# Optimization experiments

Hardware: AMD Instinct MI355X
Metric: run time of the kernel (lower is better)

The kernel has to match this reference:

```python
import jax, jax.numpy as jnp
import numpy as np
from jax import lax

C_OUT = 32   # out_capsules[0]
D_OUT = 8    # out_capsules[1]
ROUTING_ITERS = 3
EPS = 1e-8


def squash(s):
    # squash over capsule-channel axis c (dim 1 of B c d h w)
    n2 = jnp.sum(s * s, axis=1, keepdims=True)
    return s * (n2 / (1.0 + n2)) / jnp.sqrt(n2 + EPS)


def setup_inputs() -> dict:
    key = jax.random.key(0)
    k1, k2 = jax.random.split(key)
    x = jax.random.normal(k1, (8, 16, 8, 96, 96), dtype=jnp.float32)
    # torch Conv3d weight layout: (out_ch, in_ch, kD, kH, kW); scaled ~ kaiming-ish
    w_conv = jax.random.normal(k2, (C_OUT * D_OUT, 16, 1, 3, 3), dtype=jnp.float32) * 0.05
    return {"x": x, "w_conv": w_conv}


def reference(x, w_conv):
    # Conv3d, no bias, valid padding, stride 1, kernel (1,3,3)
    u = lax.conv_general_dilated(
        x, w_conv, window_strides=(1, 1, 1), padding='VALID',
        dimension_numbers=('NCDHW', 'OIDHW', 'NCDHW'))  # (B, c*d, D, h, w)
    B, _, D, h, w = u.shape
    # rearrange 'B (c d) D h w -> B c D d h w'
    u = u.reshape(B, C_OUT, D_OUT, D, h, w).transpose(0, 1, 3, 2, 4, 5)

    b = jnp.zeros((B, D, D_OUT, h, w), dtype=u.dtype)
    s = None
    for _ in range(ROUTING_ITERS):
        # softmax_3d: exp normalized over (d, h, w), keeping D
        e = jnp.exp(b)
        c = e / jnp.sum(e, axis=(2, 3, 4), keepdims=True)
        s = jnp.einsum('BDdhw,BcDdhw->Bcdhw', c, u)
        b = b + jnp.einsum('BcDdhw,Bcdhw->BDdhw', u, squash(s))
    return s
```

## Files before the change

kernel.cpp:

```cpp
#include <hip/hip_runtime.h>
#include <math.h>

#define CIN   16
#define DDEP  8
#define HIN   96
#define WIN   96
#define HOUT  94
#define WOUT  94
#define HW    (HOUT*WOUT)
#define CH    256
#define DCAP  8
#define KTOT  (CIN*9)
#define KTILES 5
#define APAD  168
#define EPSQ  1e-8f

#define B_ELEMS ((size_t)8*DDEP*DCAP*HW)
#define WFRAG_ELEMS ((size_t)KTILES*16*64*8)
#define VSITES (DCAP*HW)
#define NBLK2  277
#define XN ((size_t)8*CIN*DDEP*HIN*WIN)
#define G_BYTES ((size_t)8*VSITES*36*4)

typedef __attribute__((ext_vector_type(8))) short bf16x8;
typedef __attribute__((ext_vector_type(4))) float f32x4;

__device__ __forceinline__ ushort f2bf(float f) {
    unsigned u = __float_as_uint(f);
    return (ushort)((u + 0x7FFFu + ((u >> 16) & 1u)) >> 16);
}
__device__ __forceinline__ float bf2f(ushort h) {
    return __uint_as_float(((unsigned)h) << 16);
}

__global__ __launch_bounds__(64) void build_wfrag(
    const float* __restrict__ w, ushort* __restrict__ w_hi, ushort* __restrict__ w_lo)
{
    const int lane = threadIdx.x;
    const int nt = blockIdx.x, kt = blockIdx.y;
    const int n  = nt*16 + (lane & 15);
    const int kb = kt*32 + (lane >> 4)*8;
    size_t off = (((size_t)kt*16 + nt)*64 + lane)*8;
    for (int j = 0; j < 8; ++j) {
        int k = kb + j;
        float v = (k < KTOT) ? w[(size_t)n*KTOT + k] : 0.f;
        ushort hi = f2bf(v);
        float  r  = v - bf2f(hi);
        ushort lo = f2bf(r);
        w_hi[off + j] = hi; w_lo[off + j] = lo;
    }
}

__global__ __launch_bounds__(256) void xconvert(
    const float* __restrict__ x, ushort* __restrict__ xb)
{
    size_t i = (size_t)blockIdx.x*256 + threadIdx.x;
    if (i*4 >= XN) return;
    float4 v = ((const float4*)x)[i];
    ushort4 o;
    o.x = f2bf(v.x); o.y = f2bf(v.y); o.z = f2bf(v.z); o.w = f2bf(v.w);
    ((ushort4*)xb)[i] = o;
}

__global__ __launch_bounds__(256) void zreduce(
    const float* __restrict__ Zp, float* __restrict__ Z, int dst, int count)
{
    const int bd = blockIdx.x;
    const float* p = Zp + (size_t)bd * count;
    float s = 0.f;
    for (int i = threadIdx.x; i < count; i += 256) s += p[i];
    #pragma unroll
    for (int off = 1; off < 64; off <<= 1) s += __shfl_xor(s, off);
    __shared__ float ps[4];
    if ((threadIdx.x & 63) == 0) ps[threadIdx.x >> 6] = s;
    __syncthreads();
    if (threadIdx.x == 0) Z[dst + bd] = ps[0] + ps[1] + ps[2] + ps[3];
}

__global__ __launch_bounds__(256, 2) void conv_g(
    const ushort* __restrict__ xb,
    const ushort* __restrict__ w_hi, const ushort* __restrict__ w_lo,
    float* __restrict__ Gm)
{
    const int t  = threadIdx.x;
    const int wx = blockIdx.x, h0 = blockIdx.y, bb = blockIdx.z;
    const int w0 = wx*8;

    __shared__ __align__(16) ushort a_hi[64][APAD];
    __shared__ union {
        ushort patchb[CIN][DDEP][3][10];
        float gst[4][16][36];
    } ov;

    for (int i = t; i < CIN*DDEP*3*5; i += 256) {
        int ci = i / 120, rem = i - ci*120;
        int D  = rem / 15, r2 = rem - D*15;
        int kh = r2 / 5, uc = r2 - kh*5;
        int xc = w0 + uc*2;
        const ushort* row = xb + (((size_t)(bb*CIN + ci)*DDEP + D)*HIN + (h0+kh))*WIN;
        unsigned v;
        if (xc + 1 < WIN) v = *(const unsigned*)&row[xc];
        else { unsigned e = row[95]; v = e | (e << 16); }
        *(unsigned*)&ov.patchb[ci][D][kh][uc*2] = v;
    }
    __syncthreads();

    {
        const int site = t >> 2, kg = t & 3;
        const int D = site >> 3, wi = site & 7;
        #pragma unroll
        for (int u2 = 0; u2 < 18; ++u2) {
            int k0 = kg*36 + u2*2;
            int ci0 = k0/9, r0 = k0 - ci0*9, kh0 = r0/3, kw0 = r0 - kh0*3;
            int k1 = k0 + 1;
            int ci1 = k1/9, r1 = k1 - ci1*9, kh1 = r1/3, kw1 = r1 - kh1*3;
            unsigned lo = ov.patchb[ci0][D][kh0][wi+kw0];
            unsigned hi = ov.patchb[ci1][D][kh1][wi+kw1];
            *(unsigned*)&a_hi[site][k0] = lo | (hi << 16);
        }
        if (t < 64) {
            #pragma unroll
            for (int kk = KTOT; kk < KTILES*32; kk += 2)
                *(unsigned*)&a_hi[t][kk] = 0u;
        }
    }
    __syncthreads();

    const int wv = t >> 6, lane = t & 63;
    const int m16 = lane & 15, quad = lane >> 4;
    const int Dq  = quad >> 1;
    const int wih = quad & 1;
    f32x4 acc[4][4];
    #pragma unroll
    for (int mt = 0; mt < 4; ++mt)
        #pragma unroll
        for (int nt = 0; nt < 4; ++nt)
            acc[mt][nt] = (f32x4){0.f, 0.f, 0.f, 0.f};

    #pragma unroll
    for (int kt = 0; kt < KTILES; ++kt) {
        bf16x8 ah[4];
        #pragma unroll
        for (int mt = 0; mt < 4; ++mt)
            ah[mt] = *(const bf16x8*)&a_hi[mt*16 + m16][kt*32 + quad*8];
        #pragma unroll
        for (int nt = 0; nt < 4; ++nt) {
            size_t off = (((size_t)kt*16 + (wv*4 + nt))*64 + lane)*8;
            bf16x8 bh = *(const bf16x8*)&w_hi[off];
            bf16x8 bl = *(const bf16x8*)&w_lo[off];
            #pragma unroll
            for (int mt = 0; mt < 4; ++mt) {
                acc[mt][nt] = __builtin_amdgcn_mfma_f32_16x16x32_bf16(ah[mt], bh, acc[mt][nt], 0, 0, 0);
                acc[mt][nt] = __builtin_amdgcn_mfma_f32_16x16x32_bf16(ah[mt], bl, acc[mt][nt], 0, 0, 0);
            }
        }
    }

    {
        const int c3 = m16 >> 3;
        const int dL = m16 & 7;
        __syncthreads();
        #pragma unroll
        for (int r = 0; r < 4; ++r) {
            const int rq = r >> 1;
            float G36[36];
            #pragma unroll
            for (int j = 0; j < 36; ++j) G36[j] = 0.f;
            #pragma unroll
            for (int nt = 0; nt < 4; ++nt) {
                float u8[8];
                #pragma unroll
                for (int mt = 0; mt < 4; ++mt) {
                    float own = acc[mt][nt][r];
                    float oth = __shfl_xor(own, 32);
                    if (Dq == 0) { u8[mt*2]   = own; u8[mt*2+1] = oth; }
                    else         { u8[mt*2+1] = own; u8[mt*2]   = oth; }
                }
                if (Dq == rq) {
                    int idx = 0;
                    #pragma unroll
                    for (int D = 0; D < 8; ++D)
                        #pragma unroll
                        for (int Dp = D; Dp < 8; ++Dp) {
                            G36[idx] += u8[D]*u8[Dp];
                            ++idx;
                        }
                }
            }
            if (Dq == rq) {
                #pragma unroll
                for (int j = 0; j < 36; ++j) G36[j] += __shfl_xor(G36[j], 8);
                if (c3 == 0) {
                    #pragma unroll
                    for (int j = 0; j < 36; ++j) ov.gst[wv][dL*2 + wih][j] = G36[j];
                }
            }
            __syncthreads();
            for (int idx2 = t; idx2 < 16*36; idx2 += 256) {
                int sidx = idx2 / 36, j = idx2 - sidx*36;
                int dd = sidx >> 1, wh = sidx & 1;
                int w = w0 + wh*4 + r;
                if (w < WOUT) {
                    float gv = ov.gst[0][sidx][j] + ov.gst[1][sidx][j]
                             + ov.gst[2][sidx][j] + ov.gst[3][sidx][j];
                    size_t gsite = ((size_t)(bb*DCAP + dd)*HOUT + h0)*WOUT + w;
                    Gm[gsite*36 + j] = gv;
                }
            }
            __syncthreads();
        }
    }
}

template<int ITER>
__global__ __launch_bounds__(256) void gram_route(
    const float* __restrict__ Gm, float* __restrict__ bws,
    const float* __restrict__ Z, float* __restrict__ Zp)
{
    const int k = blockIdx.x, bb = blockIdx.y;
    const int t = threadIdx.x;
    const int local = k*256 + t;
    const bool valid = local < VSITES;
    float ez8[8];
    #pragma unroll
    for (int D = 0; D < 8; ++D) ez8[D] = 0.f;
    if (valid) {
        const int d  = local / HW;
        const int r2 = local - d*HW;
        float bv[8], cm[8];
        if (ITER == 1) {
            const float inv = 1.0f / (float)(DCAP * HW);
            #pragma unroll
            for (int D = 0; D < 8; ++D) { bv[D] = 0.f; cm[D] = inv; }
        } else {
            #pragma unroll
            for (int D = 0; D < 8; ++D) {
                bv[D] = bws[((size_t)(bb*64 + D*8 + d))*HW + r2];
                cm[D] = expf(bv[D]) * (1.0f / Z[bb*8 + D]);
            }
        }
        float g[36];
        const float4* gp = (const float4*)(Gm + (size_t)(bb*VSITES + local)*36);
        #pragma unroll
        for (int q = 0; q < 9; ++q) {
            float4 v = gp[q];
            g[q*4+0] = v.x; g[q*4+1] = v.y; g[q*4+2] = v.z; g[q*4+3] = v.w;
        }
        float tD[8];
        #pragma unroll
        for (int D = 0; D < 8; ++D) tD[D] = 0.f;
        {
            int idx = 0;
            #pragma unroll
            for (int D = 0; D < 8; ++D)
                #pragma unroll
                for (int Dp = D; Dp < 8; ++Dp) {
                    float gv = g[idx]; ++idx;
                    tD[D] += cm[Dp] * gv;
                    if (Dp != D) tD[Dp] += cm[D] * gv;
                }
        }
        float n2 = 0.f;
        #pragma unroll
        for (int D = 0; D < 8; ++D) n2 += cm[D] * tD[D];
        float fac = (n2 / (1.f + n2)) / sqrtf(n2 + EPSQ);
        #pragma unroll
        for (int D = 0; D < 8; ++D) {
            float nb = bv[D] + fac * tD[D];
            bws[((size_t)(bb*64 + D*8 + d))*HW + r2] = nb;
            ez8[D] = expf(nb);
        }
    }
    #pragma unroll
    for (int D = 0; D < 8; ++D)
        #pragma unroll
        for (int off = 1; off < 64; off <<= 1) ez8[D] += __shfl_xor(ez8[D], off);
    __shared__ float ps[4][8];
    if ((t & 63) == 0) {
        #pragma unroll
        for (int D = 0; D < 8; ++D) ps[t >> 6][D] = ez8[D];
    }
    __syncthreads();
    if (t < 8)
        Zp[((size_t)bb*8 + t)*NBLK2 + k] = ps[0][t] + ps[1][t] + ps[2][t] + ps[3][t];
}

__global__ __launch_bounds__(256, 2) void conv_s(
    const ushort* __restrict__ xb,
    const ushort* __restrict__ w_hi, const ushort* __restrict__ w_lo,
    const float* __restrict__ bws, const float* __restrict__ Z,
    float* __restrict__ out)
{
    const int t  = threadIdx.x;
    const int wx = blockIdx.x, h0 = blockIdx.y, bb = blockIdx.z;
    const int w0 = wx*8;

    __shared__ __align__(16) ushort a_hi[64][APAD];
    __shared__ float  cms[64][8];
    __shared__ float  invZ[8];
    __shared__ union {
        ushort patchb[CIN][DDEP][3][10];
        float  sout[256][8];
    } ov;

    if (t < 8) invZ[t] = 1.0f / Z[64 + bb*8 + t];
    for (int v = t; v < 512; v += 256) {
        int Dd = v >> 3, wi = v & 7;
        int w = w0 + wi;
        float bv = (w < WOUT) ? bws[((size_t)bb*64 + Dd)*HW + (size_t)h0*WOUT + w] : 0.f;
        cms[Dd][wi] = expf(bv);
    }
    for (int i = t; i < CIN*DDEP*3*5; i += 256) {
        int ci = i / 120, rem = i - ci*120;
        int D  = rem / 15, r2 = rem - D*15;
        int kh = r2 / 5, uc = r2 - kh*5;
        int xc = w0 + uc*2;
        const ushort* row = xb + (((size_t)(bb*CIN + ci)*DDEP + D)*HIN + (h0+kh))*WIN;
        unsigned v;
        if (xc + 1 < WIN) v = *(const unsigned*)&row[xc];
        else { unsigned e = row[95]; v = e | (e << 16); }
        *(unsigned*)&ov.patchb[ci][D][kh][uc*2] = v;
    }
    __syncthreads();

    {
        const int site = t >> 2, kg = t & 3;
        const int D = site >> 3, wi = site & 7;
        #pragma unroll
        for (int u2 = 0; u2 < 18; ++u2) {
            int k0 = kg*36 + u2*2;
            int ci0 = k0/9, r0 = k0 - ci0*9, kh0 = r0/3, kw0 = r0 - kh0*3;
            int k1 = k0 + 1;
            int ci1 = k1/9, r1 = k1 - ci1*9, kh1 = r1/3, kw1 = r1 - kh1*3;
            unsigned lo = ov.patchb[ci0][D][kh0][wi+kw0];
            unsigned hi = ov.patchb[ci1][D][kh1][wi+kw1];
            *(unsigned*)&a_hi[site][k0] = lo | (hi << 16);
        }
        if (t < 64) {
            #pragma unroll
            for (int kk = KTOT; kk < KTILES*32; kk += 2)
                *(unsigned*)&a_hi[t][kk] = 0u;
        }
    }
    __syncthreads();

    const int wv = t >> 6, lane = t & 63;
    const int m16 = lane & 15, quad = lane >> 4;
    f32x4 acc[4][4];
    #pragma unroll
    for (int mt = 0; mt < 4; ++mt)
        #pragma unroll
        for (int nt = 0; nt < 4; ++nt)
            acc[mt][nt] = (f32x4){0.f, 0.f, 0.f, 0.f};

    #pragma unroll
    for (int kt = 0; kt < KTILES; ++kt) {
        bf16x8 ah[4];
        #pragma unroll
        for (int mt = 0; mt < 4; ++mt)
            ah[mt] = *(const bf16x8*)&a_hi[mt*16 + m16][kt*32 + quad*8];
        #pragma unroll
        for (int nt = 0; nt < 4; ++nt) {
            size_t off = (((size_t)kt*16 + (wv*4 + nt))*64 + lane)*8;
            bf16x8 bh = *(const bf16x8*)&w_hi[off];
            bf16x8 bl = *(const bf16x8*)&w_lo[off];
            #pragma unroll
            for (int mt = 0; mt < 4; ++mt) {
                acc[mt][nt] = __builtin_amdgcn_mfma_f32_16x16x32_bf16(ah[mt], bh, acc[mt][nt], 0, 0, 0);
                acc[mt][nt] = __builtin_amdgcn_mfma_f32_16x16x32_bf16(ah[mt], bl, acc[mt][nt], 0, 0, 0);
            }
        }
    }

    const int d   = m16 & 7;
    const int Dq  = quad >> 1;
    const int wih = quad & 1;
    float svv[4][4];
    {
        float cmw[4][4];
        #pragma unroll
        for (int mt = 0; mt < 4; ++mt) {
            int D = mt*2 + Dq;
            float iz = invZ[D];
            #pragma unroll
            for (int r = 0; r < 4; ++r) cmw[mt][r] = cms[D*8 + d][wih*4 + r] * iz;
        }
        #pragma unroll
        for (int nt = 0; nt < 4; ++nt)
            #pragma unroll
            for (int r = 0; r < 4; ++r) {
                float partial = 0.f;
                #pragma unroll
                for (int mt = 0; mt < 4; ++mt) partial += cmw[mt][r]*acc[mt][nt][r];
                partial += __shfl_xor(partial, 32);
                svv[nt][r] = partial;
            }
    }
    if (quad < 2) {
        #pragma unroll
        for (int nt = 0; nt < 4; ++nt) {
            int ch = wv*64 + nt*16 + m16;
            #pragma unroll
            for (int r = 0; r < 4; ++r) ov.sout[ch][wih*4 + r] = svv[nt][r];
        }
    }
    __syncthreads();
    for (int i = t; i < 1024; i += 256) {
        int c2 = i >> 2, wip = i & 3;
        int w = w0 + wip*2;
        if (w + 1 < WOUT) {
            float2 v2 = { ov.sout[c2][wip*2], ov.sout[c2][wip*2 + 1] };
            *(float2*)&out[((size_t)bb*CH + c2)*HW + (size_t)h0*WOUT + w] = v2;
        }
    }
}

extern "C" void kernel_launch(void* const* d_in, const int* in_sizes, int n_in,
                              void* d_out, int out_size, void* d_ws, size_t ws_size,
                              hipStream_t stream)
{
    (void)in_sizes; (void)n_in; (void)out_size; (void)ws_size;
    const float* x     = (const float*)d_in[0];
    const float* wconv = (const float*)d_in[1];
    float* out = (float*)d_out;

    float*  bws  = (float*)d_ws;
    float*  Z    = bws + B_ELEMS;
    float*  Zp   = Z + 128;
    ushort* w_hi = (ushort*)(Zp + 64*NBLK2);
    ushort* w_lo = w_hi + WFRAG_ELEMS;
    ushort* xb   = w_lo + WFRAG_ELEMS;
    size_t  base = (size_t)((char*)(xb + XN) - (char*)d_ws);
    size_t  goff = (base + 255) & ~(size_t)255;
    float*  Gm   = (float*)((char*)d_ws + goff);

    const dim3 grid(12, 94, 8);
    build_wfrag<<<dim3(16, KTILES), 64, 0, stream>>>(wconv, w_hi, w_lo);
    xconvert<<<(unsigned)(XN/4/256), 256, 0, stream>>>(x, xb);
    conv_g<<<grid, 256, 0, stream>>>(xb, w_hi, w_lo, Gm);
    gram_route<1><<<dim3(NBLK2, 8), 256, 0, stream>>>(Gm, bws, Z, Zp);
    zreduce<<<64, 256, 0, stream>>>(Zp, Z, 0, NBLK2);
    gram_route<2><<<dim3(NBLK2, 8), 256, 0, stream>>>(Gm, bws, Z, Zp);
    zreduce<<<64, 256, 0, stream>>>(Zp, Z, 64, NBLK2);
    conv_s<<<grid, 256, 0, stream>>>(xb, w_hi, w_lo, bws, Z, out);
}
```

Baseline: 564.1 us.

## Fuse first routing iteration into conv_g and fold Z reductions into consumers

Merges the weight-fragment build and x-to-bf16 conversion into one prep kernel. Computes the first routing update (uniform coupling) inside conv_g from the per-site Gram values already in shared memory, and writes b and per-block exp partial sums there. This removes one full gram_route pass over Gm. The zreduce kernels are dropped; each consumer block re-sums the partials itself. The cost is redundant partial-sum reads in every block, plus extra per-block work and shared memory in conv_g.

```diff
diff --git a/kernel.cpp b/kernel.cpp
--- a/kernel.cpp
+++ b/kernel.cpp
@@ -17,9 +17,11 @@
 
 #define B_ELEMS ((size_t)8*DDEP*DCAP*HW)
 #define WFRAG_ELEMS ((size_t)KTILES*16*64*8)
+#define BLK_PER_B (94*12)
 #define VSITES (DCAP*HW)
 #define NBLK2  277
 #define XN ((size_t)8*CIN*DDEP*HIN*WIN)
+#define XBLK  9216
 #define G_BYTES ((size_t)8*VSITES*36*4)
 
 typedef __attribute__((ext_vector_type(8))) short bf16x8;
@@ -33,54 +35,39 @@
     return __uint_as_float(((unsigned)h) << 16);
 }
 
-__global__ __launch_bounds__(64) void build_wfrag(
+__global__ __launch_bounds__(256) void prep(
+    const float* __restrict__ x, ushort* __restrict__ xb,
     const float* __restrict__ w, ushort* __restrict__ w_hi, ushort* __restrict__ w_lo)
 {
-    const int lane = threadIdx.x;
-    const int nt = blockIdx.x, kt = blockIdx.y;
-    const int n  = nt*16 + (lane & 15);
-    const int kb = kt*32 + (lane >> 4)*8;
-    size_t off = (((size_t)kt*16 + nt)*64 + lane)*8;
-    for (int j = 0; j < 8; ++j) {
-        int k = kb + j;
-        float v = (k < KTOT) ? w[(size_t)n*KTOT + k] : 0.f;
-        ushort hi = f2bf(v);
-        float  r  = v - bf2f(hi);
-        ushort lo = f2bf(r);
-        w_hi[off + j] = hi; w_lo[off + j] = lo;
-    }
-}
-
-__global__ __launch_bounds__(256) void xconvert(
-    const float* __restrict__ x, ushort* __restrict__ xb)
-{
-    size_t i = (size_t)blockIdx.x*256 + threadIdx.x;
-    if (i*4 >= XN) return;
-    float4 v = ((const float4*)x)[i];
-    ushort4 o;
-    o.x = f2bf(v.x); o.y = f2bf(v.y); o.z = f2bf(v.z); o.w = f2bf(v.w);
-    ((ushort4*)xb)[i] = o;
-}
-
-__global__ __launch_bounds__(256) void zreduce(
-    const float* __restrict__ Zp, float* __restrict__ Z, int dst, int count)
-{
-    const int bd = blockIdx.x;
-    const float* p = Zp + (size_t)bd * count;
-    float s = 0.f;
-    for (int i = threadIdx.x; i < count; i += 256) s += p[i];
-    #pragma unroll
-    for (int off = 1; off < 64; off <<= 1) s += __shfl_xor(s, off);
-    __shared__ float ps[4];
-    if ((threadIdx.x & 63) == 0) ps[threadIdx.x >> 6] = s;
-    __syncthreads();
-    if (threadIdx.x == 0) Z[dst + bd] = ps[0] + ps[1] + ps[2] + ps[3];
+    const int bid = blockIdx.x;
+    if (bid < XBLK) {
+        size_t i = (size_t)bid*256 + threadIdx.x;
+        float4 v = ((const float4*)x)[i];
+        ushort4 o;
+        o.x = f2bf(v.x); o.y = f2bf(v.y); o.z = f2bf(v.z); o.w = f2bf(v.w);
+        ((ushort4*)xb)[i] = o;
+    } else if (threadIdx.x < 64) {
+        const int b2 = bid - XBLK;
+        const int nt = b2 & 15, kt = b2 >> 4;
+        const int lane = threadIdx.x;
+        const int n  = nt*16 + (lane & 15);
+        const int kb = kt*32 + (lane >> 4)*8;
+        size_t off = (((size_t)kt*16 + nt)*64 + lane)*8;
+        for (int j = 0; j < 8; ++j) {
+            int k = kb + j;
+            float v = (k < KTOT) ? w[(size_t)n*KTOT + k] : 0.f;
+            ushort hi = f2bf(v);
+            float  r  = v - bf2f(hi);
+            ushort lo = f2bf(r);
+            w_hi[off + j] = hi; w_lo[off + j] = lo;
+        }
+    }
 }
 
 __global__ __launch_bounds__(256, 2) void conv_g(
     const ushort* __restrict__ xb,
     const ushort* __restrict__ w_hi, const ushort* __restrict__ w_lo,
-    float* __restrict__ Gm)
+    float* __restrict__ bws, float* __restrict__ Zp1, float* __restrict__ Gm)
 {
     const int t  = threadIdx.x;
     const int wx = blockIdx.x, h0 = blockIdx.y, bb = blockIdx.z;
@@ -91,6 +78,7 @@
         ushort patchb[CIN][DDEP][3][10];
         float gst[4][16][36];
     } ov;
+    __shared__ float b1s[8][8][8];
 
     for (int i = t; i < CIN*DDEP*3*5; i += 256) {
         int ci = i / 120, rem = i - ci*120;
@@ -207,18 +195,78 @@
                     Gm[gsite*36 + j] = gv;
                 }
             }
+            if (t < 16) {
+                const int sdd = t >> 1, swh = t & 1;
+                const int sw = w0 + swh*4 + r;
+                if (sw < WOUT) {
+                    const float inv = 1.0f / (float)(DCAP * HW);
+                    float g36[36];
+                    #pragma unroll
+                    for (int j = 0; j < 36; ++j)
+                        g36[j] = ov.gst[0][t][j] + ov.gst[1][t][j]
+                               + ov.gst[2][t][j] + ov.gst[3][t][j];
+                    float tD[8];
+                    #pragma unroll
+                    for (int D = 0; D < 8; ++D) tD[D] = 0.f;
+                    int idx = 0;
+                    #pragma unroll
+                    for (int D = 0; D < 8; ++D)
+                        #pragma unroll
+                        for (int Dp = D; Dp < 8; ++Dp) {
+                            float gv = g36[idx]; ++idx;
+                            tD[D] += inv * gv;
+                            if (Dp != D) tD[Dp] += inv * gv;
+                        }
+                    float n2 = 0.f;
+                    #pragma unroll
+                    for (int D = 0; D < 8; ++D) n2 += inv * tD[D];
+                    float fac = (n2 / (1.f + n2)) / sqrtf(n2 + EPSQ);
+                    #pragma unroll
+                    for (int D = 0; D < 8; ++D) b1s[sdd][swh*4 + r][D] = fac * tD[D];
+                }
+            }
             __syncthreads();
         }
     }
-}
-
-template<int ITER>
-__global__ __launch_bounds__(256) void gram_route(
+
+    {
+        int Dd = t >> 2, wip = t & 3;
+        int D = Dd >> 3, d2 = Dd & 7;
+        int w = w0 + wip*2;
+        float ez = 0.f;
+        if (w + 1 < WOUT) {
+            float2 add;
+            add.x = b1s[d2][wip*2][D];
+            add.y = b1s[d2][wip*2 + 1][D];
+            *(float2*)&bws[((size_t)bb*64 + Dd)*HW + (size_t)h0*WOUT + w] = add;
+            ez = expf(add.x) + expf(add.y);
+        }
+        #pragma unroll
+        for (int off = 1; off < 32; off <<= 1) ez += __shfl_xor(ez, off);
+        if ((t & 31) == 0)
+            Zp1[((size_t)bb*8 + D)*BLK_PER_B + h0*12 + wx] = ez;
+    }
+}
+
+__global__ __launch_bounds__(256) void gram_route2(
     const float* __restrict__ Gm, float* __restrict__ bws,
-    const float* __restrict__ Z, float* __restrict__ Zp)
+    const float* __restrict__ Zp1, float* __restrict__ Zp2)
 {
     const int k = blockIdx.x, bb = blockIdx.y;
     const int t = threadIdx.x;
+
+    __shared__ float invZ1[8];
+    {
+        const int Dg = t >> 5;
+        const float* p = Zp1 + ((size_t)bb*8 + Dg)*BLK_PER_B;
+        float s = 0.f;
+        for (int k2 = (t & 31); k2 < BLK_PER_B; k2 += 32) s += p[k2];
+        #pragma unroll
+        for (int off = 1; off < 32; off <<= 1) s += __shfl_xor(s, off);
+        if ((t & 31) == 0) invZ1[Dg] = 1.0f / s;
+    }
+    __syncthreads();
+
     const int local = k*256 + t;
     const bool valid = local < VSITES;
     float ez8[8];
@@ -228,16 +276,10 @@
         const int d  = local / HW;
         const int r2 = local - d*HW;
         float bv[8], cm[8];
-        if (ITER == 1) {
-            const float inv = 1.0f / (float)(DCAP * HW);
-            #pragma unroll
-            for (int D = 0; D < 8; ++D) { bv[D] = 0.f; cm[D] = inv; }
-        } else {
-            #pragma unroll
-            for (int D = 0; D < 8; ++D) {
-                bv[D] = bws[((size_t)(bb*64 + D*8 + d))*HW + r2];
-                cm[D] = expf(bv[D]) * (1.0f / Z[bb*8 + D]);
-            }
+        #pragma unroll
+        for (int D = 0; D < 8; ++D) {
+            bv[D] = bws[((size_t)(bb*64 + D*8 + d))*HW + r2];
+            cm[D] = expf(bv[D]) * invZ1[D];
         }
         float g[36];
         const float4* gp = (const float4*)(Gm + (size_t)(bb*VSITES + local)*36);
@@ -282,13 +324,13 @@
     }
     __syncthreads();
     if (t < 8)
-        Zp[((size_t)bb*8 + t)*NBLK2 + k] = ps[0][t] + ps[1][t] + ps[2][t] + ps[3][t];
+        Zp2[((size_t)bb*8 + t)*NBLK2 + k] = ps[0][t] + ps[1][t] + ps[2][t] + ps[3][t];
 }
 
 __global__ __launch_bounds__(256, 2) void conv_s(
     const ushort* __restrict__ xb,
     const ushort* __restrict__ w_hi, const ushort* __restrict__ w_lo,
-    const float* __restrict__ bws, const float* __restrict__ Z,
+    const float* __restrict__ bws, const float* __restrict__ Zp2,
     float* __restrict__ out)
 {
     const int t  = threadIdx.x;
@@ -303,7 +345,15 @@
         float  sout[256][8];
     } ov;
 
-    if (t < 8) invZ[t] = 1.0f / Z[64 + bb*8 + t];
+    {
+        const int Dg = t >> 5;
+        const float* p = Zp2 + ((size_t)bb*8 + Dg)*NBLK2;
+        float s = 0.f;
+        for (int k2 = (t & 31); k2 < NBLK2; k2 += 32) s += p[k2];
+        #pragma unroll
+        for (int off = 1; off < 32; off <<= 1) s += __shfl_xor(s, off);
+        if ((t & 31) == 0) invZ[Dg] = 1.0f / s;
+    }
     for (int v = t; v < 512; v += 256) {
         int Dd = v >> 3, wi = v & 7;
         int w = w0 + wi;
@@ -425,9 +475,9 @@
     float* out = (float*)d_out;
 
     float*  bws  = (float*)d_ws;
-    float*  Z    = bws + B_ELEMS;
-    float*  Zp   = Z + 128;
-    ushort* w_hi = (ushort*)(Zp + 64*NBLK2);
+    float*  Zp1  = bws + B_ELEMS;
+    float*  Zp2  = Zp1 + 64*BLK_PER_B;
+    ushort* w_hi = (ushort*)(Zp2 + 64*NBLK2);
     ushort* w_lo = w_hi + WFRAG_ELEMS;
     ushort* xb   = w_lo + WFRAG_ELEMS;
     size_t  base = (size_t)((char*)(xb + XN) - (char*)d_ws);
@@ -435,12 +485,8 @@
     float*  Gm   = (float*)((char*)d_ws + goff);
 
     const dim3 grid(12, 94, 8);
-    build_wfrag<<<dim3(16, KTILES), 64, 0, stream>>>(wconv, w_hi, w_lo);
-    xconvert<<<(unsigned)(XN/4/256), 256, 0, stream>>>(x, xb);
-    conv_g<<<grid, 256, 0, stream>>>(xb, w_hi, w_lo, Gm);
-    gram_route<1><<<dim3(NBLK2, 8), 256, 0, stream>>>(Gm, bws, Z, Zp);
-    zreduce<<<64, 256, 0, stream>>>(Zp, Z, 0, NBLK2);
-    gram_route<2><<<dim3(NBLK2, 8), 256, 0, stream>>>(Gm, bws, Z, Zp);
-    zreduce<<<64, 256, 0, stream>>>(Zp, Z, 64, NBLK2);
-    conv_s<<<grid, 256, 0, stream>>>(xb, w_hi, w_lo, bws, Z, out);
-}
+    prep<<<XBLK + 80, 256, 0, stream>>>(x, xb, wconv, w_hi, w_lo);
+    conv_g<<<grid, 256, 0, stream>>>(xb, w_hi, w_lo, bws, Zp1, Gm);
+    gram_route2<<<dim3(NBLK2, 8), 256, 0, stream>>>(Gm, bws, Zp1, Zp2);
+    conv_s<<<grid, 256, 0, stream>>>(xb, w_hi, w_lo, bws, Zp2, out);
+}
```

New measurement: 644.9 us. 1.14x slower.
